# Optimization experiments

Hardware: AMD Instinct MI355X
Metric: run time of the kernel (lower is better)

## Reference

```python
import jax, jax.numpy as jnp
import numpy as np

B, N, L = 32, 50, 16384  # batch, n_templates, segment length
KT = 4096                # template kernel length


def conv1d(x, w, pad, groups=1):
    # x: [B, Cin, L], w: [Cout, Cin/groups, K] (torch layout)
    return jax.lax.conv_general_dilated(
        x, w, window_strides=(1,), padding=[(pad, pad)],
        dimension_numbers=('NCH', 'OIH', 'NCH'), feature_group_count=groups)


def maxpool3(x):
    # MaxPool1d(kernel=3, stride=3), floor mode (VALID)
    return jax.lax.reduce_window(x, -jnp.inf, jax.lax.max,
                                 (1, 1, 3), (1, 1, 3), 'VALID')


def pad_to(x, m):
    p = (-x.shape[-1]) % m
    pads = ((0, 0),) * (x.ndim - 1) + ((0, p),)
    return jnp.pad(x, pads)


def setup_inputs() -> dict:
    key = jax.random.key(0)
    ks = jax.random.split(key, 12)
    return dict(
        xi=jax.random.normal(ks[0], (B, 2, L), jnp.float32),
        S_t_m12=jax.random.normal(ks[1], (2, 1, L), jnp.float32) * 0.01,
        template=jax.random.normal(ks[2], (N, 2, KT), jnp.float32) * 0.01,
        hh_sqrt=jax.random.uniform(ks[3], (N, 2), jnp.float32) + 0.5,
        W1=jax.random.normal(ks[4], (16, 2, 3), jnp.float32) * 0.1,
        b1=jnp.zeros((16,), jnp.float32),
        W2=jax.random.normal(ks[5], (32, 16, 3), jnp.float32) * 0.1,
        b2=jnp.zeros((32,), jnp.float32),
        W3=jax.random.normal(ks[6], (32, 128), jnp.float32) * 0.1,
        b3=jnp.zeros((32,), jnp.float32),
        W4=jax.random.normal(ks[7], (2, 32), jnp.float32) * 0.1,
        b4=jnp.zeros((2,), jnp.float32),
    )


def reference(xi, S_t_m12, template, hh_sqrt, W1, b1, W2, b2, W3, b3, W4, b4):
    # Whitening matched filter: grouped conv with kernel length L
    y = conv1d(xi, S_t_m12, L - 1, groups=2)          # [B, 2, 2L-1]
    y = pad_to(y, L)                                   # [B, 2, 2L]
    # wrap-fold each channel: reshape(B,2,L).sum over the fold axis
    d_SA = y[:, 0].reshape(-1, 2, L).sum(1)[:, None, :]  # [B,1,L]
    d_SE = y[:, 1].reshape(-1, 2, L).sum(1)[:, None, :]
    h_SA = template[:, 0, :].reshape(-1, 1, KT)          # [N,1,KT]
    h_SE = template[:, 1, :].reshape(-1, 1, KT)
    dh_A = pad_to(conv1d(d_SA, h_SA, KT - 1), L).reshape(-1, N, 2, L).sum(2)  # [B,N,L]
    dh_E = pad_to(conv1d(d_SE, h_SE, KT - 1), L).reshape(-1, N, 2, L).sum(2)
    z = jnp.stack((dh_A, dh_E), -1).transpose(0, 2, 1, 3)  # [B,L,N,2]
    z = z / hh_sqrt                                         # broadcast [N,2]
    z = z.max(axis=1).transpose(0, 2, 1)                    # [B,2,N]
    # small CNN + MLP head
    h = maxpool3(jax.nn.sigmoid(conv1d(z, W1, 0) + b1[None, :, None]))  # [B,16,16]
    h = maxpool3(jax.nn.sigmoid(conv1d(h, W2, 0) + b2[None, :, None]))  # [B,32,4]
    h = h.reshape(h.shape[0], -1)                                        # [B,128]
    h = jax.nn.relu(h @ W3.T + b3)
    return h @ W4.T + b4                                                 # [B,2]
```

## Files before the change

### kernel.cpp

```cpp
#include <hip/hip_runtime.h>
#include <math.h>

#define L_LEN 16384
#define M_LEN 8192
#define KT_LEN 4096
#define BB 32
#define NTPL 50
#define SPEC_STRIDE 8224
#define NSIG 166
#define NTF 1024
#define NTI 512
#define PI_F 3.14159265358979323846f
#define C16 0.98078528040323044f
#define S16 0.19509032201612827f
#define C8 0.92387953251128674f
#define S8 0.38268343236508978f

typedef float cf2 __attribute__((ext_vector_type(2)));


__device__ __forceinline__ cf2 cmul(cf2 a, cf2 b) {
    cf2 t, d;
    asm("v_pk_mul_f32 %0, %1, %2 op_sel:[0,0] op_sel_hi:[0,1]"
        : "=v"(t) : "v"(a), "v"(b));
    asm("v_pk_fma_f32 %0, %1, %2, %3 op_sel:[1,1,0] op_sel_hi:[1,0,1] neg_lo:[0,1,0]"
        : "=v"(d) : "v"(a), "v"(b), "v"(t));
    return d;
}
__device__ __forceinline__ cf2 cmulc(cf2 a, cf2 b) {
    cf2 t, d;
    asm("v_pk_mul_f32 %0, %1, %2 op_sel:[0,0] op_sel_hi:[0,1] neg_hi:[0,1]"
        : "=v"(t) : "v"(a), "v"(b));
    asm("v_pk_fma_f32 %0, %1, %2, %3 op_sel:[1,1,0] op_sel_hi:[1,0,1]"
        : "=v"(d) : "v"(a), "v"(b), "v"(t));
    return d;
}
__device__ __forceinline__ cf2 cmulca(cf2 a, cf2 b) {
    cf2 t, d;
    asm("v_pk_mul_f32 %0, %1, %2 op_sel:[0,0] op_sel_hi:[0,1]"
        : "=v"(t) : "v"(a), "v"(b));
    asm("v_pk_fma_f32 %0, %1, %2, %3 op_sel:[1,1,0] op_sel_hi:[1,0,1] neg_hi:[1,0,0]"
        : "=v"(d) : "v"(a), "v"(b), "v"(t));
    return d;
}
__device__ __forceinline__ cf2 pk_addch(cf2 a, cf2 b) {
    cf2 d;
    asm("v_pk_add_f32 %0, %1, %2 neg_hi:[0,1]" : "=v"(d) : "v"(a), "v"(b));
    return d;
}
__device__ __forceinline__ cf2 pk_subcl(cf2 a, cf2 b) {
    cf2 d;
    asm("v_pk_add_f32 %0, %1, %2 neg_lo:[0,1]" : "=v"(d) : "v"(a), "v"(b));
    return d;
}
__device__ __forceinline__ cf2 pk_compose1(cf2 s, cf2 r) {
    cf2 d;
    asm("v_pk_add_f32 %0, %1, %2 op_sel:[0,1] op_sel_hi:[0,0] neg_lo:[0,1]"
        : "=v"(d) : "v"(s), "v"(r));
    return d;
}
__device__ __forceinline__ cf2 pk_compose2(cf2 s, cf2 r) {
    cf2 d;
    asm("v_pk_add_f32 %0, %1, %2 op_sel:[0,1] op_sel_hi:[0,0] neg_hi:[1,0]"
        : "=v"(d) : "v"(s), "v"(r));
    return d;
}
template<int SIGN>
__device__ __forceinline__ cf2 rot90(cf2 z) {
    return (SIGN < 0) ? (cf2){z.y, -z.x} : (cf2){-z.y, z.x};
}
template<int SIGN>
__device__ __forceinline__ cf2 ldT(const cf2* __restrict__ T, int idx) {
    cf2 t = T[idx];
    if (SIGN > 0) t.y = -t.y;
    return t;
}

__device__ __forceinline__ int swz(int i) { return i ^ (((i >> 5) & 15) << 1); }

__device__ __forceinline__ int pos8(int f) {
    return ((f & 7) << 10) | (((f >> 3) & 7) << 7) |
           (((f >> 6) & 7) << 4) | (((f >> 9) & 7) << 1) | ((f >> 12) & 1);
}

template<int SIGN>
__device__ __forceinline__ void dft16(cf2 x[16]) {
    const float S = (SIGN < 0) ? -1.f : 1.f;
    const cf2 w1 = {0.9238795325112867f, S * 0.3826834323650898f};
    const cf2 w2 = {0.7071067811865476f, S * 0.7071067811865476f};
    const cf2 w3 = {0.3826834323650898f, S * 0.9238795325112867f};
    cf2 v[16];
    #pragma unroll
    for (int n1 = 0; n1 < 4; ++n1) {
        cf2 a0 = x[n1], a1 = x[n1+4], a2 = x[n1+8], a3 = x[n1+12];
        cf2 t0 = a0 + a2, t2 = a0 - a2;
        cf2 t1 = a1 + a3, t3 = rot90<SIGN>(a1 - a3);
        cf2 u0 = t0 + t1, u1 = t2 + t3;
        cf2 u2 = t0 - t1, u3 = t2 - t3;
        if (n1 == 1) { u1 = cmul(u1, w1); u2 = cmul(u2, w2); u3 = cmul(u3, w3); }
        else if (n1 == 2) { u1 = cmul(u1, w2); u2 = rot90<SIGN>(u2);
                            u3 = rot90<SIGN>(cmul(u3, w2)); }
        else if (n1 == 3) { u1 = cmul(u1, w3); u2 = rot90<SIGN>(cmul(u2, w2));
                            u3 = -cmul(u3, w1); }
        v[0*4+n1] = u0; v[1*4+n1] = u1; v[2*4+n1] = u2; v[3*4+n1] = u3;
    }
    #pragma unroll
    for (int r = 0; r < 4; ++r) {
        cf2 a0 = v[r*4+0], a1 = v[r*4+1], a2 = v[r*4+2], a3 = v[r*4+3];
        cf2 t0 = a0 + a2, t2 = a0 - a2;
        cf2 t1 = a1 + a3, t3 = rot90<SIGN>(a1 - a3);
        x[r]    = t0 + t1; x[r+4]  = t2 + t3;
        x[r+8]  = t0 - t1; x[r+12] = t2 - t3;
    }
}

template<int SIGN>
__device__ __forceinline__ void butterfly16(cf2* A, const int idx[16], cf2 w1) {
    cf2 x[16];
    #pragma unroll
    for (int n = 0; n < 16; ++n) x[n] = A[idx[n]];
    dft16<SIGN>(x);
    A[idx[0]] = x[0];
    A[idx[1]] = cmul(x[1], w1);
    const cf2 w2 = cmul(w1, w1);
    A[idx[2]] = cmul(x[2], w2);
    const cf2 w3 = cmul(w1, w2);
    A[idx[3]] = cmul(x[3], w3);
    const cf2 w4 = cmul(w2, w2);
    A[idx[4]] = cmul(x[4], w4);
    A[idx[5]] = cmul(x[5], cmul(w1, w4));
    A[idx[6]] = cmul(x[6], cmul(w2, w4));
    A[idx[7]] = cmul(x[7], cmul(w3, w4));
    const cf2 w8 = cmul(w4, w4);
    A[idx[8]]  = cmul(x[8],  w8);
    A[idx[9]]  = cmul(x[9],  cmul(w1, w8));
    A[idx[10]] = cmul(x[10], cmul(w2, w8));
    A[idx[11]] = cmul(x[11], cmul(w3, w8));
    const cf2 w12 = cmul(w4, w8);
    A[idx[12]] = cmul(x[12], w12);
    A[idx[13]] = cmul(x[13], cmul(w1, w12));
    A[idx[14]] = cmul(x[14], cmul(w2, w12));
    A[idx[15]] = cmul(x[15], cmul(w3, w12));
}

template<int SIGN>
__device__ __forceinline__ void dft8(cf2 x[8]) {
    const float R2 = 0.70710678118654752f;
    const cf2 w81 = { R2, SIGN * R2 };
    const cf2 w83 = { -R2, SIGN * R2 };
    cf2 u0 = x[0] + x[4], u1 = x[1] + x[5], u2 = x[2] + x[6], u3 = x[3] + x[7];
    cf2 v0 = x[0] - x[4];
    cf2 v1 = cmul(x[1] - x[5], w81);
    cf2 v2 = rot90<SIGN>(x[2] - x[6]);
    cf2 v3 = cmul(x[3] - x[7], w83);
    cf2 t0 = u0 + u2, t2 = u0 - u2;
    cf2 t1 = u1 + u3, t3 = rot90<SIGN>(u1 - u3);
    x[0] = t0 + t1; x[2] = t2 + t3; x[4] = t0 - t1; x[6] = t2 - t3;
    cf2 s0 = v0 + v2, s2 = v0 - v2;
    cf2 s1 = v1 + v3, s3 = rot90<SIGN>(v1 - v3);
    x[1] = s0 + s1; x[3] = s2 + s3; x[5] = s0 - s1; x[7] = s2 - s3;
}

template<int SIGN>
__device__ __forceinline__ void butterfly8(cf2* A, const int idx[8], cf2 w1) {
    cf2 x[8];
    #pragma unroll
    for (int n = 0; n < 8; ++n) x[n] = A[idx[n]];
    dft8<SIGN>(x);
    A[idx[0]] = x[0];
    A[idx[1]] = cmul(x[1], w1);
    const cf2 w2 = cmul(w1, w1);
    A[idx[2]] = cmul(x[2], w2);
    const cf2 w3 = cmul(w1, w2);
    A[idx[3]] = cmul(x[3], w3);
    const cf2 w4 = cmul(w2, w2);
    A[idx[4]] = cmul(x[4], w4);
    A[idx[5]] = cmul(x[5], cmul(w1, w4));
    A[idx[6]] = cmul(x[6], cmul(w2, w4));
    A[idx[7]] = cmul(x[7], cmul(w3, w4));
}

__global__ __launch_bounds__(NTF, 4)
void fwd_fft_kernel(const float* __restrict__ xi, const float* __restrict__ w,
                    const float* __restrict__ tmpl, cf2* __restrict__ Tw,
                    cf2* __restrict__ spec) {
    __shared__ __attribute__((aligned(16))) cf2 A[M_LEN];
    const int sig = blockIdx.x;
    const int tid = threadIdx.x;

    if (sig >= NSIG) {
        const int k = (sig - NSIG) * NTF + tid;
        const int quad = k >> 12, mm = k & 4095;
        float s, c; __sincosf(PI_F * (float)mm / 8192.f, &s, &c);
        cf2 v;
        if      (quad == 0) v = (cf2){ c, -s};
        else if (quad == 1) v = (cf2){-s, -c};
        else if (quad == 2) v = (cf2){-c,  s};
        else                v = (cf2){ s,  c};
        Tw[k] = v;
        return;
    }

    const float* src;
    int nre;
    if (sig < 64)      { src = xi   + sig * L_LEN;         nre = L_LEN; }
    else if (sig < 66) { src = w    + (sig - 64) * L_LEN;  nre = L_LEN; }
    else               { src = tmpl + (sig - 66) * KT_LEN; nre = KT_LEN; }
    const bool isW = (sig >= 64 && sig < 66);
    const int nc = nre >> 1;
    const float4* s4 = (const float4*)src;
    const int g0 = tid ^ ((tid >> 4) & 15);
    #pragma unroll
    for (int m = 0; m < 4; ++m) {
        const int u = 2*tid + 2048*m;
        float4 vv = (u < nc) ? s4[tid + 1024*m] : make_float4(0.f, 0.f, 0.f, 0.f);
        ((float4*)A)[g0 + 1024*m] = vv;
    }
    __syncthreads();

    {
        int idx[8]; const int b0 = swz(tid);
        #pragma unroll
        for (int n = 0; n < 8; ++n) idx[n] = b0 + 1024*n;
        float sn, cs; __sincosf(-PI_F * (float)(2*tid) / 8192.f, &sn, &cs);
        butterfly8<-1>(A, idx, (cf2){cs, sn});
    }
    __syncthreads();
    {
        const int blk = tid >> 7, j = tid & 127, jb = blk*1024;
        const int jsw = j ^ (((j >> 5) & 3) << 1);
        int idx[8];
        #pragma unroll
        for (int n = 0; n < 8; ++n) idx[n] = jb + 128*n + (jsw ^ ((n & 3) << 3));
        float sn, cs; __sincosf(-PI_F * (float)(16*j) / 8192.f, &sn, &cs);
        butterfly8<-1>(A, idx, (cf2){cs, sn});
    }
    __syncthreads();
    {
        const int blk = tid >> 4, j = tid & 15;
        const int base = blk*128 + j, bx = (blk & 3) << 3;
        int idx[8];
        #pragma unroll
        for (int n = 0; n < 8; ++n) idx[n] = (base + 16*n) ^ bx ^ ((n >> 1) << 1);
        float sn, cs; __sincosf(-PI_F * (float)(128*j) / 8192.f, &sn, &cs);
        butterfly8<-1>(A, idx, (cf2){cs, sn});
    }
    __syncthreads();
    {
        const int blk = tid >> 1, j = tid & 1;
        const int Xa = ((blk >> 1) & 15) << 1;
        const int base = ((blk << 4) | j) ^ (Xa & 16);
        const int xv = Xa & 14;
        int idx[8];
        #pragma unroll
        for (int n = 0; n < 8; ++n) idx[n] = base + ((2*n) ^ xv);
        cf2 w1 = j ? (cf2){C8, -S8} : (cf2){1.f, 0.f};
        butterfly8<-1>(A, idx, w1);
    }
    __syncthreads();
    #pragma unroll
    for (int m = 0; m < 4; ++m) {
        float4 pq = ((float4*)A)[g0 + 1024*m];
        ((float4*)A)[g0 + 1024*m] = make_float4(pq.x + pq.z, pq.y + pq.w,
                                                pq.x - pq.z, pq.y - pq.w);
    }
    __syncthreads();

    cf2* out = spec + (size_t)sig * SPEC_STRIDE;
    #pragma unroll
    for (int m = 0; m < 8; ++m) {
        const int f = tid + 1024*m;
        const int fb = (M_LEN - f) & (M_LEN - 1);
        cf2 Za = A[swz(pos8(f))];
        cf2 Zb = A[swz(pos8(fb))];
        cf2 E = (cf2){0.5f*(Za.x + Zb.x), 0.5f*(Za.y - Zb.y)};
        cf2 D = (cf2){Za.x - Zb.x, Za.y + Zb.y};
        cf2 O = (cf2){0.5f*D.y, -0.5f*D.x};
        float sn, cs;
        __sincosf(-PI_F * (float)f / 8192.f, &sn, &cs);
        cf2 val = E + (cf2){cs*O.x - sn*O.y, cs*O.y + sn*O.x};
        if (isW) {
            const int k = (4094 * f) & (L_LEN - 1);
            float psn, pcs; __sincosf(-PI_F * (float)k / 8192.f, &psn, &pcs);
            val = cmul((cf2){val.x, -val.y}, (cf2){pcs, psn});
        }
        out[f] = val;
    }
    if (tid == 0) {
        cf2 Za = A[swz(0)];
        cf2 val = (cf2){Za.x - Za.y, 0.f};
        if (isW) {
            val = (cf2){-val.x, 0.f};
        }
        out[M_LEN] = val;
    }
}

__global__ __launch_bounds__(NTI, 4)
void inv_fft_kernel(const cf2* __restrict__ spec, const cf2* __restrict__ T,
                    const float* __restrict__ hh, float* __restrict__ zarr) {
    __shared__ __attribute__((aligned(16))) cf2 A[M_LEN];
    const int idx0 = blockIdx.x;
    const int c = idx0 & 1;
    const int n = (idx0 >> 1) % NTPL;
    const int b = idx0 / (2 * NTPL);
    const int tid = threadIdx.x;

    const cf2* Xs = spec + (size_t)(b*2 + c)      * SPEC_STRIDE;
    const cf2* Vs = spec + (size_t)(64 + c)       * SPEC_STRIDE;
    const cf2* Hs = spec + (size_t)(66 + n*2 + c) * SPEC_STRIDE;
    const float4* X4 = (const float4*)Xs;
    const float4* V4 = (const float4*)Vs;
    const float4* H4 = (const float4*)Hs;
    const float4* T4 = (const float4*)T;
    const int g0 = tid ^ ((tid >> 4) & 15);

    #pragma unroll
    for (int m = 0; m < 4; ++m) {
        const int u = 2*tid + 1024*m;
        float4 xf = X4[tid + 512*m], vf = V4[tid + 512*m], hf = H4[tid + 512*m];
        cf2 P0 = cmulc(cmul((cf2){xf.x, xf.y}, (cf2){vf.x, vf.y}), (cf2){hf.x, hf.y});
        cf2 P1 = cmulc(cmul((cf2){xf.z, xf.w}, (cf2){vf.z, vf.w}), (cf2){hf.z, hf.w});
        cf2 Q0 = cmulc(cmul(Xs[M_LEN - u],     Vs[M_LEN - u]),     Hs[M_LEN - u]);
        cf2 Q1 = cmulc(cmul(Xs[M_LEN - 1 - u], Vs[M_LEN - 1 - u]), Hs[M_LEN - 1 - u]);
        float4 tw = T4[tid + 512*m];
        cf2 t0 = (cf2){tw.x, tw.y}, t1 = (cf2){tw.z, tw.w};
        cf2 Sp0 = pk_addch(P0, Q0), Sm0 = pk_subcl(P0, Q0);
        cf2 R0 = cmulca(t0, Sm0);
        cf2 Sp1 = pk_addch(P1, Q1), Sm1 = pk_subcl(P1, Q1);
        cf2 R1 = cmulca(t1, Sm1);
        cf2 Z0 = pk_compose1(Sp0, R0);
        cf2 Z1 = pk_compose1(Sp1, R1);
        ((float4*)A)[g0 + 512*m] = make_float4(Z0.x, Z0.y, Z1.x, Z1.y);
        if (u > 0) A[swz(M_LEN - u)] = pk_compose2(Sp0, R0);
        A[swz(M_LEN - 1 - u)] = pk_compose2(Sp1, R1);
    }
    if (tid == 0) {
        cf2 S = cmulc(cmul(Xs[4096], Vs[4096]), Hs[4096]);
        A[swz(4096)] = (cf2){2.f * S.x, -2.f * S.y};
    }
    __syncthreads();

    {
        int idx[16]; const int b0 = swz(tid);
        #pragma unroll
        for (int nn = 0; nn < 16; ++nn) idx[nn] = b0 + 512*nn;
        butterfly16<+1>(A, idx, ldT<+1>(T, 2*tid));
    }
    __syncthreads();
    {
        const int blk = tid >> 5, j = tid & 31, jb = blk*512;
        int idx[16];
        #pragma unroll
        for (int nn = 0; nn < 16; ++nn) idx[nn] = jb + 32*nn + (j ^ (2*nn));
        butterfly16<+1>(A, idx, ldT<+1>(T, 32*j));
    }
    __syncthreads();
    {
        const int blk = tid >> 1, j = tid & 1;
        const int xv = (blk & 15) << 1, b3 = blk*32 + j;
        int idx[16];
        #pragma unroll
        for (int nn = 0; nn < 16; ++nn) idx[nn] = b3 + ((2*nn) ^ xv);
        cf2 w1 = j ? (cf2){C16, S16} : (cf2){1.f, 0.f};
        butterfly16<+1>(A, idx, w1);
    }
    __syncthreads();

    float mx = -INFINITY;
    #pragma unroll
    for (int m = 0; m < 8; ++m) {
        float4 pq = ((const float4*)A)[g0 + 512*m];
        mx = fmaxf(mx, fmaxf(fmaxf(pq.x + pq.z, pq.y + pq.w),
                             fmaxf(pq.x - pq.z, pq.y - pq.w)));
    }
    __syncthreads();
    for (int off = 32; off > 0; off >>= 1)
        mx = fmaxf(mx, __shfl_xor(mx, off));
    const int lane = tid & 63, wv = tid >> 6;
    float* redf = (float*)A;
    if (lane == 0) redf[wv] = mx;
    __syncthreads();
    if (tid == 0) {
        float mm = redf[0];
        for (int i = 1; i < NTI/64; ++i) mm = fmaxf(mm, redf[i]);
        zarr[(b*2 + c)*NTPL + n] = mm / (2.f * (float)M_LEN * hh[n*2 + c]);
    }
}

#define W1_OFF 0
#define B1_OFF 96
#define W2_OFF 112
#define B2_OFF 1648
#define W3_OFF 1680
#define B3_OFF 5904
#define W4_OFF 5936
#define B4_OFF 6000
#define WSM_SZ 6002

__global__ __launch_bounds__(256)
void head_kernel(const float* __restrict__ zarr,
                 const float* __restrict__ W1, const float* __restrict__ b1,
                 const float* __restrict__ W2, const float* __restrict__ b2,
                 const float* __restrict__ W3, const float* __restrict__ b3,
                 const float* __restrict__ W4, const float* __restrict__ b4,
                 float* __restrict__ out) {
    __shared__ float wsm[WSM_SZ];
    __shared__ float zl[2*NTPL];
    __shared__ float s1[16*48];
    __shared__ float p1[16*16];
    __shared__ float s2[32*14];
    __shared__ float hflat[128];
    __shared__ float h1[32];
    const int b = blockIdx.x, tid = threadIdx.x;

    for (int i = tid; i < 96;   i += 256) wsm[W1_OFF + i] = W1[i];
    if (tid < 16)                         wsm[B1_OFF + tid] = b1[tid];
    for (int i = tid; i < 1536; i += 256) wsm[W2_OFF + i] = W2[i];
    if (tid < 32)                         wsm[B2_OFF + tid] = b2[tid];
    for (int i = tid; i < 4096; i += 256)
        wsm[W3_OFF + (i >> 7)*132 + (i & 127)] = W3[i];
    if (tid < 32)                         wsm[B3_OFF + tid] = b3[tid];
    if (tid < 64)                         wsm[W4_OFF + tid] = W4[tid];
    if (tid < 2)                          wsm[B4_OFF + tid] = b4[tid];
    for (int i = tid; i < 2*NTPL; i += 256) zl[i] = zarr[b*2*NTPL + i];
    __syncthreads();

    for (int i = tid; i < 16*48; i += 256) {
        const int o = i / 48, t = i % 48;
        float acc = wsm[B1_OFF + o];
        #pragma unroll
        for (int cc = 0; cc < 2; ++cc)
            #pragma unroll
            for (int k = 0; k < 3; ++k)
                acc += zl[cc*NTPL + t + k] * wsm[W1_OFF + o*6 + cc*3 + k];
        s1[i] = 1.f / (1.f + __expf(-acc));
    }
    __syncthreads();
    for (int i = tid; i < 16*16; i += 256) {
        const int o = i / 16, u = i % 16;
        p1[i] = fmaxf(fmaxf(s1[o*48 + 3*u], s1[o*48 + 3*u+1]), s1[o*48 + 3*u+2]);
    }
    __syncthreads();
    for (int i = tid; i < 32*14; i += 256) {
        const int o = i / 14, t = i % 14;
        float acc = wsm[B2_OFF + o];
        #pragma unroll
        for (int cc = 0; cc < 16; ++cc)
            #pragma unroll
            for (int k = 0; k < 3; ++k)
                acc += p1[cc*16 + t + k] * wsm[W2_OFF + o*48 + cc*3 + k];
        s2[o*14 + t] = 1.f / (1.f + __expf(-acc));
    }
    __syncthreads();
    for (int i = tid; i < 128; i += 256) {
        const int o = i / 4, u = i % 4;
        hflat[i] = fmaxf(fmaxf(s2[o*14 + 3*u], s2[o*14 + 3*u+1]), s2[o*14 + 3*u+2]);
    }
    __syncthreads();
    {
        const int o = tid >> 3, lg = tid & 7;
        float acc = 0.f;
        #pragma unroll
        for (int k = 0; k < 16; ++k)
            acc += hflat[lg + 8*k] * wsm[W3_OFF + o*132 + lg + 8*k];
        acc += __shfl_xor(acc, 1);
        acc += __shfl_xor(acc, 2);
        acc += __shfl_xor(acc, 4);
        if (lg == 0) h1[o] = fmaxf(acc + wsm[B3_OFF + o], 0.f);
    }
    __syncthreads();
    if (tid < 64) {
        const int o = tid >> 5, j = tid & 31;
        float p = h1[j] * wsm[W4_OFF + o*32 + j];
        p += __shfl_xor(p, 1);
        p += __shfl_xor(p, 2);
        p += __shfl_xor(p, 4);
        p += __shfl_xor(p, 8);
        p += __shfl_xor(p, 16);
        if (j == 0) out[b*2 + o] = p + wsm[B4_OFF + o];
    }
}

extern "C" void kernel_launch(void* const* d_in, const int* in_sizes, int n_in,
                              void* d_out, int out_size, void* d_ws, size_t ws_size,
                              hipStream_t stream) {
    const float* xi   = (const float*)d_in[0];
    const float* Sw   = (const float*)d_in[1];
    const float* tmpl = (const float*)d_in[2];
    const float* hh   = (const float*)d_in[3];
    const float* W1   = (const float*)d_in[4];
    const float* b1   = (const float*)d_in[5];
    const float* W2   = (const float*)d_in[6];
    const float* b2   = (const float*)d_in[7];
    const float* W3   = (const float*)d_in[8];
    const float* b3   = (const float*)d_in[9];
    const float* W4   = (const float*)d_in[10];
    const float* b4   = (const float*)d_in[11];
    float* out = (float*)d_out;

    cf2* T16  = (cf2*)d_ws;
    cf2* spec = T16 + 16384;
    float* zarr = (float*)(spec + (size_t)NSIG * SPEC_STRIDE);

    fwd_fft_kernel<<<dim3(NSIG + 16), dim3(NTF), 0, stream>>>(xi, Sw, tmpl, T16, spec);
    inv_fft_kernel<<<dim3(BB * NTPL * 2), dim3(NTI), 0, stream>>>(spec, T16, hh, zarr);
    head_kernel<<<dim3(BB), dim3(256), 0, stream>>>(zarr, W1, b1, W2, b2, W3, b3, W4, b4, out);
}
```

Baseline: 153.0 us.

## Fold first inverse-FFT radix-2 stage into spectrum pre-processing and fuse last stage into max

```diff
diff --git a/kernel.cpp b/kernel.cpp
--- a/kernel.cpp
+++ b/kernel.cpp
@@ -11,10 +11,9 @@
 #define NTF 1024
 #define NTI 512
 #define PI_F 3.14159265358979323846f
-#define C16 0.98078528040323044f
-#define S16 0.19509032201612827f
 #define C8 0.92387953251128674f
 #define S8 0.38268343236508978f
+#define R2_F 0.70710678118654752f
 
 typedef float cf2 __attribute__((ext_vector_type(2)));
 
@@ -145,9 +144,8 @@
 
 template<int SIGN>
 __device__ __forceinline__ void dft8(cf2 x[8]) {
-    const float R2 = 0.70710678118654752f;
-    const cf2 w81 = { R2, SIGN * R2 };
-    const cf2 w83 = { -R2, SIGN * R2 };
+    const cf2 w81 = { R2_F, SIGN * R2_F };
+    const cf2 w83 = { -R2_F, SIGN * R2_F };
     cf2 u0 = x[0] + x[4], u1 = x[1] + x[5], u2 = x[2] + x[6], u3 = x[3] + x[7];
     cf2 v0 = x[0] - x[4];
     cf2 v1 = cmul(x[1] - x[5], w81);
@@ -313,66 +311,113 @@
     const float4* V4 = (const float4*)Vs;
     const float4* H4 = (const float4*)Hs;
     const float4* T4 = (const float4*)T;
-    const int g0 = tid ^ ((tid >> 4) & 15);
-
-    #pragma unroll
-    for (int m = 0; m < 4; ++m) {
-        const int u = 2*tid + 1024*m;
-        float4 xf = X4[tid + 512*m], vf = V4[tid + 512*m], hf = H4[tid + 512*m];
-        cf2 P0 = cmulc(cmul((cf2){xf.x, xf.y}, (cf2){vf.x, vf.y}), (cf2){hf.x, hf.y});
-        cf2 P1 = cmulc(cmul((cf2){xf.z, xf.w}, (cf2){vf.z, vf.w}), (cf2){hf.z, hf.w});
-        cf2 Q0 = cmulc(cmul(Xs[M_LEN - u],     Vs[M_LEN - u]),     Hs[M_LEN - u]);
-        cf2 Q1 = cmulc(cmul(Xs[M_LEN - 1 - u], Vs[M_LEN - 1 - u]), Hs[M_LEN - 1 - u]);
-        float4 tw = T4[tid + 512*m];
-        cf2 t0 = (cf2){tw.x, tw.y}, t1 = (cf2){tw.z, tw.w};
-        cf2 Sp0 = pk_addch(P0, Q0), Sm0 = pk_subcl(P0, Q0);
-        cf2 R0 = cmulca(t0, Sm0);
-        cf2 Sp1 = pk_addch(P1, Q1), Sm1 = pk_subcl(P1, Q1);
-        cf2 R1 = cmulca(t1, Sm1);
-        cf2 Z0 = pk_compose1(Sp0, R0);
-        cf2 Z1 = pk_compose1(Sp1, R1);
-        ((float4*)A)[g0 + 512*m] = make_float4(Z0.x, Z0.y, Z1.x, Z1.y);
-        if (u > 0) A[swz(M_LEN - u)] = pk_compose2(Sp0, R0);
-        A[swz(M_LEN - 1 - u)] = pk_compose2(Sp1, R1);
+
+    #pragma unroll
+    for (int m = 0; m < 2; ++m) {
+        const int tp = tid + 512*m;
+        const int f0 = 2*tp, f1 = f0 + 1;
+        float4 xa = X4[tp],        va = V4[tp],        ha = H4[tp];
+        float4 xq = X4[tp + 2048], vq = V4[tp + 2048], hq = H4[tp + 2048];
+        cf2 PA0 = cmulc(cmul((cf2){xa.x, xa.y}, (cf2){va.x, va.y}), (cf2){ha.x, ha.y});
+        cf2 PA1 = cmulc(cmul((cf2){xa.z, xa.w}, (cf2){va.z, va.w}), (cf2){ha.z, ha.w});
+        cf2 QB0 = cmulc(cmul((cf2){xq.x, xq.y}, (cf2){vq.x, vq.y}), (cf2){hq.x, hq.y});
+        cf2 QB1 = cmulc(cmul((cf2){xq.z, xq.w}, (cf2){vq.z, vq.w}), (cf2){hq.z, hq.w});
+        cf2 PB0 = cmulc(cmul(Xs[4096 - f0], Vs[4096 - f0]), Hs[4096 - f0]);
+        cf2 PB1 = cmulc(cmul(Xs[4096 - f1], Vs[4096 - f1]), Hs[4096 - f1]);
+        cf2 QA0 = cmulc(cmul(Xs[8192 - f0], Vs[8192 - f0]), Hs[8192 - f0]);
+        cf2 QA1 = cmulc(cmul(Xs[8192 - f1], Vs[8192 - f1]), Hs[8192 - f1]);
+        float4 tf4 = T4[tp];
+        float4 t2a = T4[2*tp];
+        float4 t2b = T4[2*tp + 1];
+        cf2 Tf0 = (cf2){tf4.x, tf4.y}, Tf1 = (cf2){tf4.z, tf4.w};
+        cf2 T20 = (cf2){t2a.x, t2a.y}, T21 = (cf2){t2b.x, t2b.y};
+        cf2 SpA0 = pk_addch(PA0, QA0), SmA0 = pk_subcl(PA0, QA0);
+        cf2 RA0 = cmulca(Tf0, SmA0);
+        cf2 ZA1_0 = pk_compose1(SpA0, RA0);
+        cf2 ZA2_0 = pk_compose2(SpA0, RA0);
+        cf2 tB0 = (cf2){-Tf0.y, -Tf0.x};
+        cf2 SpB0 = pk_addch(PB0, QB0), SmB0 = pk_subcl(PB0, QB0);
+        cf2 RB0 = cmulca(tB0, SmB0);
+        cf2 ZB1_0 = pk_compose1(SpB0, RB0);
+        cf2 ZB2_0 = pk_compose2(SpB0, RB0);
+        cf2 top0 = ZA1_0 + ZB2_0;
+        cf2 bot0 = cmulca(T20, ZA1_0 - ZB2_0);
+        cf2 SpA1 = pk_addch(PA1, QA1), SmA1 = pk_subcl(PA1, QA1);
+        cf2 RA1 = cmulca(Tf1, SmA1);
+        cf2 ZA1_1 = pk_compose1(SpA1, RA1);
+        cf2 ZA2_1 = pk_compose2(SpA1, RA1);
+        cf2 tB1 = (cf2){-Tf1.y, -Tf1.x};
+        cf2 SpB1 = pk_addch(PB1, QB1), SmB1 = pk_subcl(PB1, QB1);
+        cf2 RB1 = cmulca(tB1, SmB1);
+        cf2 ZB1_1 = pk_compose1(SpB1, RB1);
+        cf2 ZB2_1 = pk_compose2(SpB1, RB1);
+        cf2 top1 = ZA1_1 + ZB2_1;
+        cf2 bot1 = cmulca(T21, ZA1_1 - ZB2_1);
+        const int gt = tp ^ ((tp >> 4) & 15);
+        ((float4*)A)[gt]        = make_float4(top0.x, top0.y, top1.x, top1.y);
+        ((float4*)A)[2048 + gt] = make_float4(bot0.x, bot0.y, bot1.x, bot1.y);
+        if (tp > 0) {
+            cf2 tr0 = ZB1_0 + ZA2_0;
+            cf2 dr0 = cmul(ZB1_0 - ZA2_0, T20);
+            A[swz(4096 - f0)] = tr0;
+            A[swz(8192 - f0)] = -dr0;
+        }
+        cf2 tr1 = ZB1_1 + ZA2_1;
+        cf2 dr1 = cmul(ZB1_1 - ZA2_1, T21);
+        A[swz(4096 - f1)] = tr1;
+        A[swz(8192 - f1)] = -dr1;
     }
     if (tid == 0) {
-        cf2 S = cmulc(cmul(Xs[4096], Vs[4096]), Hs[4096]);
-        A[swz(4096)] = (cf2){2.f * S.x, -2.f * S.y};
-    }
-    __syncthreads();
-
-    {
-        int idx[16]; const int b0 = swz(tid);
-        #pragma unroll
-        for (int nn = 0; nn < 16; ++nn) idx[nn] = b0 + 512*nn;
-        butterfly16<+1>(A, idx, ldT<+1>(T, 2*tid));
-    }
-    __syncthreads();
-    {
-        const int blk = tid >> 5, j = tid & 31, jb = blk*512;
+        cf2 P = cmulc(cmul(Xs[2048], Vs[2048]), Hs[2048]);
+        cf2 Q = cmulc(cmul(Xs[6144], Vs[6144]), Hs[6144]);
+        cf2 Tc = (cf2){R2_F, -R2_F};
+        cf2 Sp = pk_addch(P, Q), Sm = pk_subcl(P, Q);
+        cf2 R = cmulca(Tc, Sm);
+        cf2 Z1 = pk_compose1(Sp, R), Z2 = pk_compose2(Sp, R);
+        cf2 d = Z1 - Z2;
+        A[swz(2048)] = Z1 + Z2;
+        A[swz(6144)] = (cf2){-d.y, d.x};
+    }
+    __syncthreads();
+
+    {
+        const int h = tid >> 8, j = tid & 255;
+        const int Hb = h << 12;
+        const int jx = j ^ (((j >> 5) & 7) << 1);
         int idx[16];
         #pragma unroll
-        for (int nn = 0; nn < 16; ++nn) idx[nn] = jb + 32*nn + (j ^ (2*nn));
-        butterfly16<+1>(A, idx, ldT<+1>(T, 32*j));
-    }
-    __syncthreads();
-    {
-        const int blk = tid >> 1, j = tid & 1;
-        const int xv = (blk & 15) << 1, b3 = blk*32 + j;
+        for (int nn = 0; nn < 16; ++nn)
+            idx[nn] = Hb + 256*nn + (jx ^ ((nn & 1) << 4));
+        butterfly16<+1>(A, idx, ldT<+1>(T, 4*j));
+    }
+    __syncthreads();
+    {
+        const int h = tid >> 8, q = (tid >> 4) & 15, j = tid & 15;
+        const int base = (h << 12) + (q << 8);
+        const int qb = q & 1;
         int idx[16];
         #pragma unroll
-        for (int nn = 0; nn < 16; ++nn) idx[nn] = b3 + ((2*nn) ^ xv);
-        cf2 w1 = j ? (cf2){C16, S16} : (cf2){1.f, 0.f};
-        butterfly16<+1>(A, idx, w1);
+        for (int nn = 0; nn < 16; ++nn)
+            idx[nn] = base + 16*(nn ^ qb) + (j ^ (((nn >> 1) & 7) << 1));
+        butterfly16<+1>(A, idx, ldT<+1>(T, 64*j));
     }
     __syncthreads();
 
     float mx = -INFINITY;
-    #pragma unroll
-    for (int m = 0; m < 8; ++m) {
-        float4 pq = ((const float4*)A)[g0 + 512*m];
-        mx = fmaxf(mx, fmaxf(fmaxf(pq.x + pq.z, pq.y + pq.w),
-                             fmaxf(pq.x - pq.z, pq.y - pq.w)));
+    {
+        const int bb = 16 * (tid ^ ((tid >> 4) & 1));
+        const int m3 = ((tid >> 1) & 7) << 1;
+        cf2 x[16];
+        #pragma unroll
+        for (int e = 0; e < 8; ++e) {
+            float4 v = ((const float4*)A)[(bb + ((2*e) ^ m3)) >> 1];
+            x[2*e]     = (cf2){v.x, v.y};
+            x[2*e + 1] = (cf2){v.z, v.w};
+        }
+        dft16<+1>(x);
+        #pragma unroll
+        for (int nn = 0; nn < 16; ++nn)
+            mx = fmaxf(mx, fmaxf(x[nn].x, x[nn].y));
     }
     __syncthreads();
     for (int off = 32; off > 0; off >>= 1)
```

Measured after the change: 154.5 us. About the same (+1.0%).
